# Performance work log

Measured on AMD Instinct MI355X. Metric: run time of the kernel, lower is better.

Reference implementation:

```python
import jax, jax.numpy as jnp
from jax import lax
import numpy as np

B, C, T = 128, 64, 750
NOUT, K, HID = 4, 16, 128


def _conv(x, w, b=None):
    y = lax.conv_general_dilated(x, w, (1, 1), 'VALID', dimension_numbers=('NCHW', 'OIHW', 'NCHW'))
    return y if b is None else y + b[None, :, None, None]


def _bn(x, g, b, m, v):
    s = g / jnp.sqrt(v + 1e-5)
    return (x - m[None, :, None, None]) * s[None, :, None, None] + b[None, :, None, None]


def _pool(x):
    return lax.reduce_window(x, -jnp.inf, lax.max, (1, 1, 3, 1), (1, 1, 3, 1), 'VALID')


def _backbone(x, ct_w, ct_b, cs_w, bn1, c2_w, bn2, c3_w, bn3, c4_w, bn4, fc_w, fc_b):
    # x: (B, C, T) -> (B, 1, T, C)  (braindecode transpose_time_to_spat)
    h = jnp.transpose(x, (0, 2, 1))[:, None]
    h = _conv(h, ct_w, ct_b)              # (B,25,T-9,C)
    h = _conv(h, cs_w)                    # (B,25,T-9,1)
    h = _pool(jax.nn.elu(_bn(h, *bn1)))   # (B,25,247,1)
    h = _pool(jax.nn.elu(_bn(_conv(h, c2_w), *bn2)))  # (B,50,79,1)
    h = _pool(jax.nn.elu(_bn(_conv(h, c3_w), *bn3)))  # (B,100,23,1)
    h = _pool(jax.nn.elu(_bn(_conv(h, c4_w), *bn4)))  # (B,200,4,1)
    h = _conv(h, fc_w, fc_b)              # (B,NOUT,1,1)
    return h[:, :, 0, 0]                  # (B,NOUT)


def _heads(feats, cluster_ids, hW1, hb1, hW2, hb2):
    # gather per-sample head params, batched small GEMMs (MoE-style dispatch)
    h = jax.nn.relu(jnp.einsum('bf,bfh->bh', feats, hW1[cluster_ids]) + hb1[cluster_ids])
    return jnp.einsum('bh,bho->bo', h, hW2[cluster_ids]) + hb2[cluster_ids]


def setup_inputs() -> dict:
    key = jax.random.key(0)
    ks = jax.random.split(key, 40)
    n = lambda i, shape, s=0.1: jax.random.normal(ks[i], shape, dtype=jnp.float32) * s
    u = lambda i, shape: jax.random.uniform(ks[i], shape, dtype=jnp.float32) + 0.5
    inp = {
        'x': n(0, (B, C, T), 1.0),
        'cluster_ids': jax.random.randint(ks[1], (B,), 0, K),
        'ct_w': n(2, (25, 1, 10, 1)), 'ct_b': n(3, (25,)),
        'cs_w': n(4, (25, 25, 1, C)),
        'bn1_g': u(5, (25,)), 'bn1_b': n(6, (25,)), 'bn1_m': n(7, (25,)), 'bn1_v': u(8, (25,)),
        'c2_w': n(9, (50, 25, 10, 1)),
        'bn2_g': u(10, (50,)), 'bn2_b': n(11, (50,)), 'bn2_m': n(12, (50,)), 'bn2_v': u(13, (50,)),
        'c3_w': n(14, (100, 50, 10, 1)),
        'bn3_g': u(15, (100,)), 'bn3_b': n(16, (100,)), 'bn3_m': n(17, (100,)), 'bn3_v': u(18, (100,)),
        'c4_w': n(19, (200, 100, 10, 1)),
        'bn4_g': u(20, (200,)), 'bn4_b': n(21, (200,)), 'bn4_m': n(22, (200,)), 'bn4_v': u(23, (200,)),
        'fc_w': n(24, (NOUT, 200, 4, 1)), 'fc_b': n(25, (NOUT,)),
        'hW1': n(26, (K, NOUT, HID)), 'hb1': n(27, (K, HID)),
        'hW2': n(28, (K, HID, NOUT)), 'hb2': n(29, (K, NOUT)),
    }
    return inp


def reference(x, cluster_ids, ct_w, ct_b, cs_w,
              bn1_g, bn1_b, bn1_m, bn1_v, c2_w,
              bn2_g, bn2_b, bn2_m, bn2_v, c3_w,
              bn3_g, bn3_b, bn3_m, bn3_v, c4_w,
              bn4_g, bn4_b, bn4_m, bn4_v, fc_w, fc_b,
              hW1, hb1, hW2, hb2):
    feats = _backbone(x, ct_w, ct_b, cs_w,
                      (bn1_g, bn1_b, bn1_m, bn1_v), c2_w,
                      (bn2_g, bn2_b, bn2_m, bn2_v), c3_w,
                      (bn3_g, bn3_b, bn3_m, bn3_v), c4_w,
                      (bn4_g, bn4_b, bn4_m, bn4_v), fc_w, fc_b)
    return _heads(feats, cluster_ids, hW1, hb1, hW2, hb2)
```

## Files before the change

### kernel.cpp

```cpp
#include <hip/hip_runtime.h>
#include <hip/hip_bf16.h>
#include <math.h>

typedef __attribute__((ext_vector_type(8))) short short8v;
typedef __attribute__((ext_vector_type(4))) float f32x4;

#define F_S1 0
#define F_H1 32
#define F_S2 64
#define F_H2 128
#define F_S3 192
#define F_H3 320
#define F_S4 448
#define F_H4 704
#define F_B1 960
#define F_P4 1024
#define F_END (1024 + 128*200*4)
#define H_BASE (F_END*2)
#define H_P1  H_BASE
#define H_WA1 (H_P1 + 128*8192)
#define H_WA2 (H_WA1 + 32*640)
#define H_WA3 (H_WA2 + 64*320)
#define H_WA4 (H_WA3 + 112*640)
#define H_P2  (H_WA4 + 208*1280)
#define H_P3  (H_P2 + 79*128*64)

#define N_WA1 (32*640)
#define N_WA2 (64*320)
#define N_WA3 (112*640)
#define N_WA4 (208*1280)
#define N_WTOT (N_WA1 + N_WA2 + N_WA3 + N_WA4)

__device__ __forceinline__ float eluf(float v) {
    return v > 0.f ? v : (expf(v) - 1.f);
}
__device__ __forceinline__ float ldh(const __hip_bfloat16* p) { return __bfloat162float(*p); }
__device__ __forceinline__ unsigned short bfb(float v) {
    __hip_bfloat16 h = __float2bfloat16(v);
    return reinterpret_cast<unsigned short&>(h);
}
__device__ __forceinline__ void ld4f(const float* p, float* v) {
    float2 a = *(const float2*)p, c = *(const float2*)(p + 2);
    v[0] = a.x; v[1] = a.y; v[2] = c.x; v[3] = c.y;
}

__global__ __launch_bounds__(256) void k_pre2(
    const float* __restrict__ ct_w, const float* __restrict__ ct_b,
    const float* __restrict__ cs_w,
    const float* __restrict__ g1, const float* __restrict__ b1,
    const float* __restrict__ m1, const float* __restrict__ v1,
    const float* __restrict__ w2,
    const float* __restrict__ g2, const float* __restrict__ b2,
    const float* __restrict__ m2, const float* __restrict__ v2,
    const float* __restrict__ w3,
    const float* __restrict__ g3, const float* __restrict__ b3,
    const float* __restrict__ m3, const float* __restrict__ v3,
    const float* __restrict__ w4,
    const float* __restrict__ g4, const float* __restrict__ b4,
    const float* __restrict__ m4, const float* __restrict__ v4,
    float* __restrict__ ws) {
    __hip_bfloat16* wsh = (__hip_bfloat16*)ws;
    int t = blockIdx.x * 256 + threadIdx.x;
    if (t < N_WA1) {
        int o = t / 640, kv = t - o * 640, kk = kv / 64, c = kv - kk * 64;
        float s = 0.f;
        if (o < 25)
            for (int i = 0; i < 25; ++i)
                s += cs_w[(o * 25 + i) * 64 + c] * ct_w[i * 10 + kk];
        wsh[H_WA1 + t] = __float2bfloat16(s);
    } else if (t < N_WA1 + N_WA2) {
        int u = t - N_WA1;
        int o = u / 320, kv = u - o * 320, kk = kv / 32, c = kv - kk * 32;
        float s = (o < 50 && c < 25) ? w2[(o * 25 + c) * 10 + kk] : 0.f;
        wsh[H_WA2 + u] = __float2bfloat16(s);
    } else if (t < N_WA1 + N_WA2 + N_WA3) {
        int u = t - N_WA1 - N_WA2;
        int o = u / 640, kv = u - o * 640, kk = kv / 64, c = kv - kk * 64;
        float s = (o < 100 && c < 50) ? w3[(o * 50 + c) * 10 + kk] : 0.f;
        wsh[H_WA3 + u] = __float2bfloat16(s);
    } else if (t < N_WTOT) {
        int u = t - N_WA1 - N_WA2 - N_WA3;
        int o = u / 1280, kv = u - o * 1280, kk = kv / 128, c = kv - kk * 128;
        float s = (o < 200 && c < 100) ? w4[(o * 100 + c) * 10 + kk] : 0.f;
        wsh[H_WA4 + u] = __float2bfloat16(s);
    } else {
        int j = t - N_WTOT;
        if (j < 25) {
            float sc = g1[j] / sqrtf(v1[j] + 1e-5f);
            ws[F_S1 + j] = sc; ws[F_H1 + j] = b1[j] - m1[j] * sc;
        } else if (j >= 32 && j < 82) {
            int ch = j - 32;
            float sc = g2[ch] / sqrtf(v2[ch] + 1e-5f);
            ws[F_S2 + ch] = sc; ws[F_H2 + ch] = b2[ch] - m2[ch] * sc;
        } else if (j >= 96 && j < 196) {
            int ch = j - 96;
            float sc = g3[ch] / sqrtf(v3[ch] + 1e-5f);
            ws[F_S3 + ch] = sc; ws[F_H3 + ch] = b3[ch] - m3[ch] * sc;
        } else if (j >= 224 && j < 424) {
            int ch = j - 224;
            float sc = g4[ch] / sqrtf(v4[ch] + 1e-5f);
            ws[F_S4 + ch] = sc; ws[F_H4 + ch] = b4[ch] - m4[ch] * sc;
        } else if (j >= 448 && j < 473) {
            int o = j - 448;
            float s = 0.f;
            for (int i = 0; i < 25; ++i) {
                float cs = 0.f;
                for (int c = 0; c < 64; ++c) cs += cs_w[(o * 25 + i) * 64 + c];
                s += cs * ct_b[i];
            }
            ws[F_B1 + o] = s;
        }
    }
}

__global__ __launch_bounds__(256) void k_conv1(
    const float* __restrict__ x, float* __restrict__ ws) {
    __hip_bfloat16* wsh = (__hip_bfloat16*)ws;
    const __hip_bfloat16* Wa = wsh + H_WA1;
    int bx = blockIdx.x, b = blockIdx.y;
    int tp0 = bx * 42;
    int PTb = min(42, 247 - tp0);
    int t0 = 126 * bx;

    __shared__ __align__(16) __hip_bfloat16 xb[144 * 64];
    __shared__ __align__(16) __hip_bfloat16 eb[32 * 128];

    for (int f = threadIdx.x; f < 64 * 36; f += 256) {
        int c = f / 36, j = f - c * 36;
        int t = t0 + 4 * j;
        const float* src = x + ((size_t)b * 64 + c) * 750 + t;
        float v[4];
        if (t + 3 < 750) {
            ld4f(src, v);
        } else {
#pragma unroll
            for (int e = 0; e < 4; ++e) v[e] = (t + e < 750) ? src[e] : 0.f;
        }
#pragma unroll
        for (int e = 0; e < 4; ++e) {
            int r = 4 * j + e;
            xb[r * 64 + (c ^ (8 * (r & 7)))] = __float2bfloat16(v[e]);
        }
    }
    __syncthreads();

    int lane = threadIdx.x & 63, wid = threadIdx.x >> 6;
    int lo = lane & 15, kg = lane >> 4;
    int ot = wid >> 1, ctg = wid & 1;
    const short8v* Ap = (const short8v*)(Wa + (size_t)(ot * 16 + lo) * 640);
    f32x4 acc[4];
#pragma unroll
    for (int q = 0; q < 4; ++q) acc[q] = (f32x4){0.f, 0.f, 0.f, 0.f};
#pragma unroll 1
    for (int sb = 0; sb < 20; sb += 10) {
        short8v af[10];
#pragma unroll
        for (int u = 0; u < 10; ++u) af[u] = Ap[(sb + u) * 4 + kg];
#pragma unroll
        for (int u = 0; u < 10; ++u) {
            int s = sb + u;
            int kk = s >> 1, cb = s & 1;
#pragma unroll
            for (int q = 0; q < 4; ++q) {
                int r = (ctg * 4 + q) * 16 + lo + kk;
                int cs = (cb * 32 + kg * 8) ^ (8 * (r & 7));
                short8v bf = *(const short8v*)&xb[r * 64 + cs];
                acc[q] = __builtin_amdgcn_mfma_f32_16x16x32_bf16(af[u], bf, acc[q], 0, 0, 0);
            }
        }
    }
#pragma unroll
    for (int q = 0; q < 4; ++q) {
        int tloc = (ctg * 4 + q) * 16 + lo;
#pragma unroll
        for (int e = 0; e < 4; ++e) {
            int o2 = ot * 16 + kg * 4 + e;
            float a = acc[q][e] + ws[F_B1 + o2];
            eb[o2 * 128 + tloc] = __float2bfloat16(eluf(a * ws[F_S1 + o2] + ws[F_H1 + o2]));
        }
    }
    __syncthreads();

    __hip_bfloat16* p1g = wsh + H_P1;
    for (int i = threadIdx.x; i < 8 * 42; i += 256) {
        int og = i / 42, pl = i - og * 42;
        if (pl < PTb) {
            int tp = tp0 + pl;
            unsigned short uv[4];
#pragma unroll
            for (int j = 0; j < 4; ++j) {
                int o = og * 4 + j;
                float v = 0.f;
                if (o < 25) {
                    const __hip_bfloat16* ep = eb + o * 128 + 3 * pl;
                    v = fmaxf(fmaxf(ldh(ep), ldh(ep + 1)), ldh(ep + 2));
                }
                uv[j] = bfb(v);
            }
            uint2 pk = {(unsigned)uv[0] | ((unsigned)uv[1] << 16),
                        (unsigned)uv[2] | ((unsigned)uv[3] << 16)};
            *(uint2*)(p1g + (size_t)tp * 4096 + b * 32 + og * 4) = pk;
        }
    }
}

__global__ __launch_bounds__(256) void k_gemm2(float* __restrict__ ws) {
    __hip_bfloat16* wsh = (__hip_bfloat16*)ws;
    const __hip_bfloat16* p1 = wsh + H_P1;
    const __hip_bfloat16* W = wsh + H_WA2;
    __hip_bfloat16* p2 = wsh + H_P2;
    int w = blockIdx.x * 4 + (threadIdx.x >> 6);
    int lane = threadIdx.x & 63, lo = lane & 15, kg = lane >> 4;
    int tp = w >> 3, s0 = (w & 7) * 16;

    const __hip_bfloat16* bbase = p1 + (size_t)(s0 + lo) * 32 + kg * 8;
    short8v B[12];
#pragma unroll
    for (int v = 0; v < 12; ++v)
        B[v] = *(const short8v*)(bbase + (size_t)(3 * tp + v) * 4096);

    f32x4 acc[4][3];
#pragma unroll
    for (int ot = 0; ot < 4; ++ot)
#pragma unroll
        for (int u = 0; u < 3; ++u) acc[ot][u] = (f32x4){0.f, 0.f, 0.f, 0.f};

#pragma unroll
    for (int ot = 0; ot < 4; ++ot) {
        const __hip_bfloat16* arow = W + (size_t)(ot * 16 + lo) * 320 + kg * 8;
#pragma unroll
        for (int kk = 0; kk < 10; ++kk) {
            short8v a = *(const short8v*)(arow + kk * 32);
#pragma unroll
            for (int u = 0; u < 3; ++u)
                acc[ot][u] = __builtin_amdgcn_mfma_f32_16x16x32_bf16(a, B[kk + u], acc[ot][u], 0, 0, 0);
        }
    }

    __hip_bfloat16* obase = p2 + (size_t)(tp * 128 + s0 + lo) * 64;
#pragma unroll
    for (int ot = 0; ot < 4; ++ot) {
        unsigned short uv[4];
#pragma unroll
        for (int e = 0; e < 4; ++e) {
            int o2 = ot * 16 + kg * 4 + e;
            float m = fmaxf(fmaxf(acc[ot][0][e], acc[ot][1][e]), acc[ot][2][e]);
            float val = (o2 < 50) ? eluf(m * ws[F_S2 + o2] + ws[F_H2 + o2]) : 0.f;
            uv[e] = bfb(val);
        }
        uint2 pk = {(unsigned)uv[0] | ((unsigned)uv[1] << 16),
                    (unsigned)uv[2] | ((unsigned)uv[3] << 16)};
        *(uint2*)(obase + ot * 16 + kg * 4) = pk;
    }
}

__global__ __launch_bounds__(256) void k_gemm3(float* __restrict__ ws) {
    __hip_bfloat16* wsh = (__hip_bfloat16*)ws;
    const __hip_bfloat16* p2 = wsh + H_P2;
    const __hip_bfloat16* W = wsh + H_WA3;
    __hip_bfloat16* p3 = wsh + H_P3;
    int w = blockIdx.x * 4 + (threadIdx.x >> 6);
    int lane = threadIdx.x & 63, lo = lane & 15, kg = lane >> 4;
    int col = w >> 1, oz = w & 1;
    int tp = col >> 3, s0 = (col & 7) * 16;

    const __hip_bfloat16* bbase = p2 + (size_t)(s0 + lo) * 64 + kg * 8;
    f32x4 acc[4][3];
#pragma unroll
    for (int ot = 0; ot < 4; ++ot)
#pragma unroll
        for (int u = 0; u < 3; ++u) acc[ot][u] = (f32x4){0.f, 0.f, 0.f, 0.f};

#pragma unroll
    for (int cb = 0; cb < 2; ++cb) {
        short8v B[12];
#pragma unroll
        for (int v = 0; v < 12; ++v)
            B[v] = *(const short8v*)(bbase + (size_t)(3 * tp + v) * 8192 + cb * 32);
#pragma unroll
        for (int ot = 0; ot < 4; ++ot) {
            if (oz && ot == 3) continue;
            const __hip_bfloat16* arow =
                W + (size_t)(oz * 64 + ot * 16 + lo) * 640 + cb * 32 + kg * 8;
#pragma unroll
            for (int kk = 0; kk < 10; ++kk) {
                short8v a = *(const short8v*)(arow + kk * 64);
#pragma unroll
                for (int u = 0; u < 3; ++u)
                    acc[ot][u] = __builtin_amdgcn_mfma_f32_16x16x32_bf16(a, B[kk + u], acc[ot][u], 0, 0, 0);
            }
        }
    }

    __hip_bfloat16* obase = p3 + (size_t)(tp * 128 + s0 + lo) * 128;
#pragma unroll
    for (int ot = 0; ot < 4; ++ot) {
        unsigned short uv[4];
#pragma unroll
        for (int e = 0; e < 4; ++e) {
            int o2 = oz * 64 + ot * 16 + kg * 4 + e;
            float val = 0.f;
            if (o2 < 100) {
                float m = fmaxf(fmaxf(acc[ot][0][e], acc[ot][1][e]), acc[ot][2][e]);
                val = eluf(m * ws[F_S3 + o2] + ws[F_H3 + o2]);
            }
            uv[e] = bfb(val);
        }
        uint2 pk = {(unsigned)uv[0] | ((unsigned)uv[1] << 16),
                    (unsigned)uv[2] | ((unsigned)uv[3] << 16)};
        *(uint2*)(obase + oz * 64 + ot * 16 + kg * 4) = pk;
    }
}

__global__ __launch_bounds__(256) void k_gemm4(float* __restrict__ ws) {
    __hip_bfloat16* wsh = (__hip_bfloat16*)ws;
    const __hip_bfloat16* p3 = wsh + H_P3;
    const __hip_bfloat16* W = wsh + H_WA4;
    float* p4 = ws + F_P4;
    int w = blockIdx.x * 4 + (threadIdx.x >> 6);
    int lane = threadIdx.x & 63, lo = lane & 15, kg = lane >> 4;
    int ot = w >> 5, ct = w & 31;
    int tp = ct >> 3, s0 = (ct & 7) * 16;

    const __hip_bfloat16* bbase = p3 + (size_t)(s0 + lo) * 128 + kg * 8;
    const __hip_bfloat16* arow0 = W + (size_t)(ot * 16 + lo) * 1280 + kg * 8;
    f32x4 acc[3];
#pragma unroll
    for (int u = 0; u < 3; ++u) acc[u] = (f32x4){0.f, 0.f, 0.f, 0.f};

#pragma unroll
    for (int cb = 0; cb < 4; ++cb) {
        short8v B[12];
#pragma unroll
        for (int v = 0; v < 12; ++v)
            B[v] = *(const short8v*)(bbase + (size_t)(3 * tp + v) * 16384 + cb * 32);
        const __hip_bfloat16* arow = arow0 + cb * 32;
#pragma unroll
        for (int kk = 0; kk < 10; ++kk) {
            short8v a = *(const short8v*)(arow + kk * 128);
#pragma unroll
            for (int u = 0; u < 3; ++u)
                acc[u] = __builtin_amdgcn_mfma_f32_16x16x32_bf16(a, B[kk + u], acc[u], 0, 0, 0);
        }
    }

#pragma unroll
    for (int e = 0; e < 4; ++e) {
        int o2 = ot * 16 + kg * 4 + e;
        if (o2 < 200) {
            float m = fmaxf(fmaxf(acc[0][e], acc[1][e]), acc[2][e]);
            p4[((size_t)(s0 + lo) * 200 + o2) * 4 + tp] =
                eluf(m * ws[F_S4 + o2] + ws[F_H4 + o2]);
        }
    }
}

__global__ __launch_bounds__(128) void k_heads(
    const float* __restrict__ ws,
    const float* __restrict__ fcw, const float* __restrict__ fcb,
    const int* __restrict__ cids,
    const float* __restrict__ hW1, const float* __restrict__ hb1,
    const float* __restrict__ hW2, const float* __restrict__ hb2,
    float* __restrict__ out) {
    const float* p4 = ws + F_P4;
    __shared__ float red[4][128];
    __shared__ float fs[4];
    int b = blockIdx.x, j = threadIdx.x;

    float pa[4] = {0.f, 0.f, 0.f, 0.f};
    for (int c = j; c < 200; c += 128) {
        const float* pp = p4 + ((size_t)b * 200 + c) * 4;
        float v0 = pp[0], v1 = pp[1], v2 = pp[2], v3 = pp[3];
#pragma unroll
        for (int o = 0; o < 4; ++o) {
            const float* fw = fcw + (o * 200 + c) * 4;
            pa[o] += fw[0] * v0 + fw[1] * v1 + fw[2] * v2 + fw[3] * v3;
        }
    }
#pragma unroll
    for (int o = 0; o < 4; ++o) red[o][j] = pa[o];
    __syncthreads();
    for (int s = 64; s > 0; s >>= 1) {
        if (j < s) {
#pragma unroll
            for (int o = 0; o < 4; ++o) red[o][j] += red[o][j + s];
        }
        __syncthreads();
    }
    if (j < 4) fs[j] = red[j][0] + fcb[j];
    __syncthreads();

    int cid = cids[b];
    float hvv = hb1[cid * 128 + j];
#pragma unroll
    for (int f = 0; f < 4; ++f) hvv += fs[f] * hW1[(cid * 4 + f) * 128 + j];
    hvv = fmaxf(hvv, 0.f);
#pragma unroll
    for (int o = 0; o < 4; ++o) red[o][j] = hvv * hW2[(cid * 128 + j) * 4 + o];
    __syncthreads();
    for (int s = 64; s > 0; s >>= 1) {
        if (j < s) {
#pragma unroll
            for (int o = 0; o < 4; ++o) red[o][j] += red[o][j + s];
        }
        __syncthreads();
    }
    if (j < 4) out[b * 4 + j] = red[j][0] + hb2[cid * 4 + j];
}

extern "C" void kernel_launch(void* const* d_in, const int* in_sizes, int n_in,
                              void* d_out, int out_size, void* d_ws, size_t ws_size,
                              hipStream_t stream) {
    (void)in_sizes; (void)n_in; (void)out_size; (void)ws_size;
    const float* x    = (const float*)d_in[0];
    const int*   cid  = (const int*)d_in[1];
    const float* ctw  = (const float*)d_in[2];
    const float* ctb  = (const float*)d_in[3];
    const float* csw  = (const float*)d_in[4];
    const float* g1 = (const float*)d_in[5],  *b1 = (const float*)d_in[6];
    const float* m1 = (const float*)d_in[7],  *v1 = (const float*)d_in[8];
    const float* w2 = (const float*)d_in[9];
    const float* g2 = (const float*)d_in[10], *b2 = (const float*)d_in[11];
    const float* m2 = (const float*)d_in[12], *v2 = (const float*)d_in[13];
    const float* w3 = (const float*)d_in[14];
    const float* g3 = (const float*)d_in[15], *b3 = (const float*)d_in[16];
    const float* m3 = (const float*)d_in[17], *v3 = (const float*)d_in[18];
    const float* w4 = (const float*)d_in[19];
    const float* g4 = (const float*)d_in[20], *b4 = (const float*)d_in[21];
    const float* m4 = (const float*)d_in[22], *v4 = (const float*)d_in[23];
    const float* fcw = (const float*)d_in[24], *fcb = (const float*)d_in[25];
    const float* hW1 = (const float*)d_in[26], *hb1 = (const float*)d_in[27];
    const float* hW2 = (const float*)d_in[28], *hb2 = (const float*)d_in[29];
    float* ws  = (float*)d_ws;
    float* out = (float*)d_out;

    k_pre2<<<dim3((N_WTOT + 512 + 255) / 256), dim3(256), 0, stream>>>(
        ctw, ctb, csw, g1, b1, m1, v1, w2, g2, b2, m2, v2,
        w3, g3, b3, m3, v3, w4, g4, b4, m4, v4, ws);
    k_conv1<<<dim3(6, 128), dim3(256), 0, stream>>>(x, ws);
    k_gemm2<<<dim3(158), dim3(256), 0, stream>>>(ws);
    k_gemm3<<<dim3(92),  dim3(256), 0, stream>>>(ws);
    k_gemm4<<<dim3(104), dim3(256), 0, stream>>>(ws);
    k_heads<<<dim3(128), dim3(128), 0, stream>>>(ws, fcw, fcb, cid,
                                                 hW1, hb1, hW2, hb2, out);
}
```

Before: 95.93 us.

## Fuse weight prep into conv1, split gemm2 finer, fold heads into gemm4

Merges the weight-prep kernel and conv1 into one launch: conv blocks rebuild the combined temporal-spatial conv1 weights in shared memory, while extra blocks convert the later-layer weights. Gemm2 now has each wave compute two output tiles, which doubles the block count. The FC and MoE heads are folded into gemm4 through a last-block-done atomic counter. The goal is to cut launch count and serial dependencies, at the cost of every conv block recomputing the conv1 weights and the heads running on a single block.

Result: slower. 151.7 us (+58.1%).

```diff
diff --git a/kernel.cpp b/kernel.cpp
--- a/kernel.cpp
+++ b/kernel.cpp
@@ -5,31 +5,30 @@
 typedef __attribute__((ext_vector_type(8))) short short8v;
 typedef __attribute__((ext_vector_type(4))) float f32x4;
 
-#define F_S1 0
-#define F_H1 32
 #define F_S2 64
 #define F_H2 128
 #define F_S3 192
 #define F_H3 320
 #define F_S4 448
 #define F_H4 704
-#define F_B1 960
+#define F_BAR 1008
 #define F_P4 1024
 #define F_END (1024 + 128*200*4)
 #define H_BASE (F_END*2)
 #define H_P1  H_BASE
-#define H_WA1 (H_P1 + 128*8192)
-#define H_WA2 (H_WA1 + 32*640)
+#define H_WA2 (H_P1 + 128*8192)
 #define H_WA3 (H_WA2 + 64*320)
 #define H_WA4 (H_WA3 + 112*640)
 #define H_P2  (H_WA4 + 208*1280)
 #define H_P3  (H_P2 + 79*128*64)
 
-#define N_WA1 (32*640)
 #define N_WA2 (64*320)
 #define N_WA3 (112*640)
 #define N_WA4 (208*1280)
-#define N_WTOT (N_WA1 + N_WA2 + N_WA3 + N_WA4)
+#define N234  (N_WA2 + N_WA3 + N_WA4)
+
+#define CONV_BLOCKS 768
+#define CVT_BLOCKS  1402
 
 __device__ __forceinline__ float eluf(float v) {
     return v > 0.f ? v : (expf(v) - 1.f);
@@ -44,7 +43,8 @@
     v[0] = a.x; v[1] = a.y; v[2] = c.x; v[3] = c.y;
 }
 
-__global__ __launch_bounds__(256) void k_pre2(
+__global__ __launch_bounds__(256) void k_front(
+    const float* __restrict__ x,
     const float* __restrict__ ct_w, const float* __restrict__ ct_b,
     const float* __restrict__ cs_w,
     const float* __restrict__ g1, const float* __restrict__ b1,
@@ -60,72 +60,94 @@
     const float* __restrict__ m4, const float* __restrict__ v4,
     float* __restrict__ ws) {
     __hip_bfloat16* wsh = (__hip_bfloat16*)ws;
-    int t = blockIdx.x * 256 + threadIdx.x;
-    if (t < N_WA1) {
-        int o = t / 640, kv = t - o * 640, kk = kv / 64, c = kv - kk * 64;
-        float s = 0.f;
-        if (o < 25)
-            for (int i = 0; i < 25; ++i)
-                s += cs_w[(o * 25 + i) * 64 + c] * ct_w[i * 10 + kk];
-        wsh[H_WA1 + t] = __float2bfloat16(s);
-    } else if (t < N_WA1 + N_WA2) {
-        int u = t - N_WA1;
-        int o = u / 320, kv = u - o * 320, kk = kv / 32, c = kv - kk * 32;
-        float s = (o < 50 && c < 25) ? w2[(o * 25 + c) * 10 + kk] : 0.f;
-        wsh[H_WA2 + u] = __float2bfloat16(s);
-    } else if (t < N_WA1 + N_WA2 + N_WA3) {
-        int u = t - N_WA1 - N_WA2;
-        int o = u / 640, kv = u - o * 640, kk = kv / 64, c = kv - kk * 64;
-        float s = (o < 100 && c < 50) ? w3[(o * 50 + c) * 10 + kk] : 0.f;
-        wsh[H_WA3 + u] = __float2bfloat16(s);
-    } else if (t < N_WTOT) {
-        int u = t - N_WA1 - N_WA2 - N_WA3;
-        int o = u / 1280, kv = u - o * 1280, kk = kv / 128, c = kv - kk * 128;
-        float s = (o < 200 && c < 100) ? w4[(o * 100 + c) * 10 + kk] : 0.f;
-        wsh[H_WA4 + u] = __float2bfloat16(s);
-    } else {
-        int j = t - N_WTOT;
-        if (j < 25) {
-            float sc = g1[j] / sqrtf(v1[j] + 1e-5f);
-            ws[F_S1 + j] = sc; ws[F_H1 + j] = b1[j] - m1[j] * sc;
-        } else if (j >= 32 && j < 82) {
-            int ch = j - 32;
-            float sc = g2[ch] / sqrtf(v2[ch] + 1e-5f);
-            ws[F_S2 + ch] = sc; ws[F_H2 + ch] = b2[ch] - m2[ch] * sc;
-        } else if (j >= 96 && j < 196) {
-            int ch = j - 96;
-            float sc = g3[ch] / sqrtf(v3[ch] + 1e-5f);
-            ws[F_S3 + ch] = sc; ws[F_H3 + ch] = b3[ch] - m3[ch] * sc;
-        } else if (j >= 224 && j < 424) {
-            int ch = j - 224;
-            float sc = g4[ch] / sqrtf(v4[ch] + 1e-5f);
-            ws[F_S4 + ch] = sc; ws[F_H4 + ch] = b4[ch] - m4[ch] * sc;
-        } else if (j >= 448 && j < 473) {
-            int o = j - 448;
+    int bx = blockIdx.x, tid = threadIdx.x;
+
+    if (bx >= CONV_BLOCKS) {
+        if (bx == CONV_BLOCKS && tid == 0) {
+            unsigned* cnt = (unsigned*)(ws + F_BAR);
+            __hip_atomic_store(cnt, 0u, __ATOMIC_RELAXED, __HIP_MEMORY_SCOPE_AGENT);
+        }
+        int u = (bx - CONV_BLOCKS) * 256 + tid;
+        if (u < N_WA2) {
+            int o = u / 320, kv = u - o * 320, kk = kv / 32, c = kv - kk * 32;
+            float s = (o < 50 && c < 25) ? w2[(o * 25 + c) * 10 + kk] : 0.f;
+            wsh[H_WA2 + u] = __float2bfloat16(s);
+        } else if (u < N_WA2 + N_WA3) {
+            int v = u - N_WA2;
+            int o = v / 640, kv = v - o * 640, kk = kv / 64, c = kv - kk * 64;
+            float s = (o < 100 && c < 50) ? w3[(o * 50 + c) * 10 + kk] : 0.f;
+            wsh[H_WA3 + v] = __float2bfloat16(s);
+        } else if (u < N234) {
+            int v = u - N_WA2 - N_WA3;
+            int o = v / 1280, kv = v - o * 1280, kk = kv / 128, c = kv - kk * 128;
+            float s = (o < 200 && c < 100) ? w4[(o * 100 + c) * 10 + kk] : 0.f;
+            wsh[H_WA4 + v] = __float2bfloat16(s);
+        } else {
+            int j = u - N234;
+            if (j < 50) {
+                float sc = g2[j] / sqrtf(v2[j] + 1e-5f);
+                ws[F_S2 + j] = sc; ws[F_H2 + j] = b2[j] - m2[j] * sc;
+            } else if (j >= 64 && j < 164) {
+                int ch = j - 64;
+                float sc = g3[ch] / sqrtf(v3[ch] + 1e-5f);
+                ws[F_S3 + ch] = sc; ws[F_H3 + ch] = b3[ch] - m3[ch] * sc;
+            } else if (j >= 192 && j < 392) {
+                int ch = j - 192;
+                float sc = g4[ch] / sqrtf(v4[ch] + 1e-5f);
+                ws[F_S4 + ch] = sc; ws[F_H4 + ch] = b4[ch] - m4[ch] * sc;
+            }
+        }
+        return;
+    }
+
+    int b = bx / 6, sub = bx % 6;
+    int tp0 = sub * 42;
+    int PTb = min(42, 247 - tp0);
+    int t0 = 126 * sub;
+    int lane = tid & 63, wid = tid >> 6;
+    int lo = lane & 15, kg = lane >> 4;
+
+    __shared__ __align__(16) __hip_bfloat16 wa1[32 * 640];
+    __shared__ __align__(16) __hip_bfloat16 xb[144 * 64];
+    __shared__ float ctl[250];
+    __shared__ float ctbl[25];
+    __shared__ float s1l[32], h1l[32], b1l[32];
+    __hip_bfloat16* eb = xb;
+
+    if (tid < 250) ctl[tid] = ct_w[tid];
+    if (tid >= 256 - 25) ctbl[tid - (256 - 25)] = ct_b[tid - (256 - 25)];
+    if (tid < 32) {
+        b1l[tid] = 0.f;
+        float sc = 0.f, hh = 0.f;
+        if (tid < 25) {
+            sc = g1[tid] / sqrtf(v1[tid] + 1e-5f);
+            hh = b1[tid] - m1[tid] * sc;
+        }
+        s1l[tid] = sc; h1l[tid] = hh;
+    }
+    for (int e = tid; e < 7 * 640; e += 256)
+        wa1[25 * 640 + e] = __float2bfloat16(0.f);
+    __syncthreads();
+
+    for (int p = tid; p < 1600; p += 256) {
+        int o = p >> 6, c = p & 63;
+        float cw[25];
+#pragma unroll
+        for (int i = 0; i < 25; ++i) cw[i] = cs_w[(o * 25 + i) * 64 + c];
+        float tb = 0.f;
+#pragma unroll
+        for (int i = 0; i < 25; ++i) tb += cw[i] * ctbl[i];
+        atomicAdd(&b1l[o], tb);
+        int omask = 8 * (o & 7);
+#pragma unroll
+        for (int kk = 0; kk < 10; ++kk) {
             float s = 0.f;
-            for (int i = 0; i < 25; ++i) {
-                float cs = 0.f;
-                for (int c = 0; c < 64; ++c) cs += cs_w[(o * 25 + i) * 64 + c];
-                s += cs * ct_b[i];
-            }
-            ws[F_B1 + o] = s;
-        }
-    }
-}
-
-__global__ __launch_bounds__(256) void k_conv1(
-    const float* __restrict__ x, float* __restrict__ ws) {
-    __hip_bfloat16* wsh = (__hip_bfloat16*)ws;
-    const __hip_bfloat16* Wa = wsh + H_WA1;
-    int bx = blockIdx.x, b = blockIdx.y;
-    int tp0 = bx * 42;
-    int PTb = min(42, 247 - tp0);
-    int t0 = 126 * bx;
-
-    __shared__ __align__(16) __hip_bfloat16 xb[144 * 64];
-    __shared__ __align__(16) __hip_bfloat16 eb[32 * 128];
-
-    for (int f = threadIdx.x; f < 64 * 36; f += 256) {
+#pragma unroll
+            for (int i = 0; i < 25; ++i) s += cw[i] * ctl[i * 10 + kk];
+            wa1[o * 640 + ((kk * 64 + c) ^ omask)] = __float2bfloat16(s);
+        }
+    }
+    for (int f = tid; f < 64 * 36; f += 256) {
         int c = f / 36, j = f - c * 36;
         int t = t0 + 4 * j;
         const float* src = x + ((size_t)b * 64 + c) * 750 + t;
@@ -144,10 +166,9 @@
     }
     __syncthreads();
 
-    int lane = threadIdx.x & 63, wid = threadIdx.x >> 6;
-    int lo = lane & 15, kg = lane >> 4;
     int ot = wid >> 1, ctg = wid & 1;
-    const short8v* Ap = (const short8v*)(Wa + (size_t)(ot * 16 + lo) * 640);
+    const __hip_bfloat16* Arow = wa1 + (ot * 16 + lo) * 640;
+    int amask = 8 * (lo & 7);
     f32x4 acc[4];
 #pragma unroll
     for (int q = 0; q < 4; ++q) acc[q] = (f32x4){0.f, 0.f, 0.f, 0.f};
@@ -155,7 +176,8 @@
     for (int sb = 0; sb < 20; sb += 10) {
         short8v af[10];
 #pragma unroll
-        for (int u = 0; u < 10; ++u) af[u] = Ap[(sb + u) * 4 + kg];
+        for (int u = 0; u < 10; ++u)
+            af[u] = *(const short8v*)&Arow[(((sb + u) * 32 + kg * 8)) ^ amask];
 #pragma unroll
         for (int u = 0; u < 10; ++u) {
             int s = sb + u;
@@ -169,21 +191,23 @@
             }
         }
     }
+    __syncthreads();
+
 #pragma unroll
     for (int q = 0; q < 4; ++q) {
         int tloc = (ctg * 4 + q) * 16 + lo;
 #pragma unroll
         for (int e = 0; e < 4; ++e) {
             int o2 = ot * 16 + kg * 4 + e;
-            float a = acc[q][e] + ws[F_B1 + o2];
-            eb[o2 * 128 + tloc] = __float2bfloat16(eluf(a * ws[F_S1 + o2] + ws[F_H1 + o2]));
+            float a = acc[q][e] + b1l[o2];
+            eb[o2 * 128 + tloc] = __float2bfloat16(eluf(a * s1l[o2] + h1l[o2]));
         }
     }
     __syncthreads();
 
     __hip_bfloat16* p1g = wsh + H_P1;
-    for (int i = threadIdx.x; i < 8 * 42; i += 256) {
-        int og = i / 42, pl = i - og * 42;
+    for (int i = tid; i < 42 * 8; i += 256) {
+        int pl = i >> 3, og = i & 7;
         if (pl < PTb) {
             int tp = tp0 + pl;
             unsigned short uv[4];
@@ -211,46 +235,38 @@
     __hip_bfloat16* p2 = wsh + H_P2;
     int w = blockIdx.x * 4 + (threadIdx.x >> 6);
     int lane = threadIdx.x & 63, lo = lane & 15, kg = lane >> 4;
-    int tp = w >> 3, s0 = (w & 7) * 16;
+    int otp = w & 1, cw = w >> 1;
+    int tp = cw >> 3, s0 = (cw & 7) * 16;
 
     const __hip_bfloat16* bbase = p1 + (size_t)(s0 + lo) * 32 + kg * 8;
     short8v B[12];
 #pragma unroll
     for (int v = 0; v < 12; ++v)
         B[v] = *(const short8v*)(bbase + (size_t)(3 * tp + v) * 4096);
-
-    f32x4 acc[4][3];
-#pragma unroll
-    for (int ot = 0; ot < 4; ++ot)
-#pragma unroll
-        for (int u = 0; u < 3; ++u) acc[ot][u] = (f32x4){0.f, 0.f, 0.f, 0.f};
-
-#pragma unroll
-    for (int ot = 0; ot < 4; ++ot) {
+#pragma unroll
+    for (int oi = 0; oi < 2; ++oi) {
+        int ot = otp * 2 + oi;
+        f32x4 acc[3];
+#pragma unroll
+        for (int u = 0; u < 3; ++u) acc[u] = (f32x4){0.f, 0.f, 0.f, 0.f};
         const __hip_bfloat16* arow = W + (size_t)(ot * 16 + lo) * 320 + kg * 8;
 #pragma unroll
         for (int kk = 0; kk < 10; ++kk) {
             short8v a = *(const short8v*)(arow + kk * 32);
 #pragma unroll
             for (int u = 0; u < 3; ++u)
-                acc[ot][u] = __builtin_amdgcn_mfma_f32_16x16x32_bf16(a, B[kk + u], acc[ot][u], 0, 0, 0);
-        }
-    }
-
-    __hip_bfloat16* obase = p2 + (size_t)(tp * 128 + s0 + lo) * 64;
-#pragma unroll
-    for (int ot = 0; ot < 4; ++ot) {
+                acc[u] = __builtin_amdgcn_mfma_f32_16x16x32_bf16(a, B[kk + u], acc[u], 0, 0, 0);
+        }
         unsigned short uv[4];
 #pragma unroll
         for (int e = 0; e < 4; ++e) {
             int o2 = ot * 16 + kg * 4 + e;
-            float m = fmaxf(fmaxf(acc[ot][0][e], acc[ot][1][e]), acc[ot][2][e]);
-            float val = (o2 < 50) ? eluf(m * ws[F_S2 + o2] + ws[F_H2 + o2]) : 0.f;
-            uv[e] = bfb(val);
+            float m = fmaxf(fmaxf(acc[0][e], acc[1][e]), acc[2][e]);
+            uv[e] = bfb((o2 < 50) ? eluf(m * ws[F_S2 + o2] + ws[F_H2 + o2]) : 0.f);
         }
         uint2 pk = {(unsigned)uv[0] | ((unsigned)uv[1] << 16),
                     (unsigned)uv[2] | ((unsigned)uv[3] << 16)};
-        *(uint2*)(obase + ot * 16 + kg * 4) = pk;
+        *(uint2*)(p2 + (size_t)(tp * 128 + s0 + lo) * 64 + ot * 16 + kg * 4) = pk;
     }
 }
 
@@ -312,100 +328,98 @@
     }
 }
 
-__global__ __launch_bounds__(256) void k_gemm4(float* __restrict__ ws) {
+__global__ __launch_bounds__(256) void k_gemm4h(
+    float* __restrict__ ws, const int* __restrict__ cids,
+    const float* __restrict__ fcw, const float* __restrict__ fcb,
+    const float* __restrict__ hW1, const float* __restrict__ hb1,
+    const float* __restrict__ hW2, const float* __restrict__ hb2,
+    float* __restrict__ out) {
     __hip_bfloat16* wsh = (__hip_bfloat16*)ws;
     const __hip_bfloat16* p3 = wsh + H_P3;
     const __hip_bfloat16* W = wsh + H_WA4;
     float* p4 = ws + F_P4;
-    int w = blockIdx.x * 4 + (threadIdx.x >> 6);
-    int lane = threadIdx.x & 63, lo = lane & 15, kg = lane >> 4;
-    int ot = w >> 5, ct = w & 31;
-    int tp = ct >> 3, s0 = (ct & 7) * 16;
-
-    const __hip_bfloat16* bbase = p3 + (size_t)(s0 + lo) * 128 + kg * 8;
-    const __hip_bfloat16* arow0 = W + (size_t)(ot * 16 + lo) * 1280 + kg * 8;
-    f32x4 acc[3];
-#pragma unroll
-    for (int u = 0; u < 3; ++u) acc[u] = (f32x4){0.f, 0.f, 0.f, 0.f};
-
-#pragma unroll
-    for (int cb = 0; cb < 4; ++cb) {
-        short8v B[12];
-#pragma unroll
-        for (int v = 0; v < 12; ++v)
-            B[v] = *(const short8v*)(bbase + (size_t)(3 * tp + v) * 16384 + cb * 32);
-        const __hip_bfloat16* arow = arow0 + cb * 32;
-#pragma unroll
-        for (int kk = 0; kk < 10; ++kk) {
-            short8v a = *(const short8v*)(arow + kk * 128);
-#pragma unroll
-            for (int u = 0; u < 3; ++u)
-                acc[u] = __builtin_amdgcn_mfma_f32_16x16x32_bf16(a, B[kk + u], acc[u], 0, 0, 0);
-        }
-    }
-
-#pragma unroll
-    for (int e = 0; e < 4; ++e) {
-        int o2 = ot * 16 + kg * 4 + e;
-        if (o2 < 200) {
-            float m = fmaxf(fmaxf(acc[0][e], acc[1][e]), acc[2][e]);
-            p4[((size_t)(s0 + lo) * 200 + o2) * 4 + tp] =
-                eluf(m * ws[F_S4 + o2] + ws[F_H4 + o2]);
-        }
-    }
-}
-
-__global__ __launch_bounds__(128) void k_heads(
-    const float* __restrict__ ws,
-    const float* __restrict__ fcw, const float* __restrict__ fcb,
-    const int* __restrict__ cids,
-    const float* __restrict__ hW1, const float* __restrict__ hb1,
-    const float* __restrict__ hW2, const float* __restrict__ hb2,
-    float* __restrict__ out) {
-    const float* p4 = ws + F_P4;
-    __shared__ float red[4][128];
-    __shared__ float fs[4];
-    int b = blockIdx.x, j = threadIdx.x;
-
-    float pa[4] = {0.f, 0.f, 0.f, 0.f};
-    for (int c = j; c < 200; c += 128) {
-        const float* pp = p4 + ((size_t)b * 200 + c) * 4;
-        float v0 = pp[0], v1 = pp[1], v2 = pp[2], v3 = pp[3];
-#pragma unroll
-        for (int o = 0; o < 4; ++o) {
-            const float* fw = fcw + (o * 200 + c) * 4;
-            pa[o] += fw[0] * v0 + fw[1] * v1 + fw[2] * v2 + fw[3] * v3;
-        }
-    }
-#pragma unroll
-    for (int o = 0; o < 4; ++o) red[o][j] = pa[o];
-    __syncthreads();
-    for (int s = 64; s > 0; s >>= 1) {
-        if (j < s) {
-#pragma unroll
-            for (int o = 0; o < 4; ++o) red[o][j] += red[o][j + s];
-        }
-        __syncthreads();
-    }
-    if (j < 4) fs[j] = red[j][0] + fcb[j];
-    __syncthreads();
-
-    int cid = cids[b];
-    float hvv = hb1[cid * 128 + j];
-#pragma unroll
-    for (int f = 0; f < 4; ++f) hvv += fs[f] * hW1[(cid * 4 + f) * 128 + j];
-    hvv = fmaxf(hvv, 0.f);
-#pragma unroll
-    for (int o = 0; o < 4; ++o) red[o][j] = hvv * hW2[(cid * 128 + j) * 4 + o];
-    __syncthreads();
-    for (int s = 64; s > 0; s >>= 1) {
-        if (j < s) {
-#pragma unroll
-            for (int o = 0; o < 4; ++o) red[o][j] += red[o][j + s];
-        }
-        __syncthreads();
-    }
-    if (j < 4) out[b * 4 + j] = red[j][0] + hb2[cid * 4 + j];
+    int tid = threadIdx.x;
+    int w = blockIdx.x * 4 + (tid >> 6);
+    int lane = tid & 63, lo = lane & 15, kg = lane >> 4;
+    {
+        int ot = w >> 5, ct = w & 31;
+        int tp = ct >> 3, s0 = (ct & 7) * 16;
+        const __hip_bfloat16* bbase = p3 + (size_t)(s0 + lo) * 128 + kg * 8;
+        const __hip_bfloat16* arow0 = W + (size_t)(ot * 16 + lo) * 1280 + kg * 8;
+        f32x4 acc[3];
+#pragma unroll
+        for (int u = 0; u < 3; ++u) acc[u] = (f32x4){0.f, 0.f, 0.f, 0.f};
+#pragma unroll
+        for (int cb = 0; cb < 4; ++cb) {
+            short8v B[12];
+#pragma unroll
+            for (int v = 0; v < 12; ++v)
+                B[v] = *(const short8v*)(bbase + (size_t)(3 * tp + v) * 16384 + cb * 32);
+            const __hip_bfloat16* arow = arow0 + cb * 32;
+#pragma unroll
+            for (int kk = 0; kk < 10; ++kk) {
+                short8v a = *(const short8v*)(arow + kk * 128);
+#pragma unroll
+                for (int u = 0; u < 3; ++u)
+                    acc[u] = __builtin_amdgcn_mfma_f32_16x16x32_bf16(a, B[kk + u], acc[u], 0, 0, 0);
+            }
+        }
+#pragma unroll
+        for (int e = 0; e < 4; ++e) {
+            int o2 = ot * 16 + kg * 4 + e;
+            if (o2 < 200) {
+                float m = fmaxf(fmaxf(acc[0][e], acc[1][e]), acc[2][e]);
+                p4[((size_t)(s0 + lo) * 200 + o2) * 4 + tp] =
+                    eluf(m * ws[F_S4 + o2] + ws[F_H4 + o2]);
+            }
+        }
+    }
+
+    __shared__ unsigned lastFlag;
+    __syncthreads();
+    if (tid == 0) {
+        unsigned* cnt = (unsigned*)(ws + F_BAR);
+        unsigned v = __hip_atomic_fetch_add(cnt, 1u, __ATOMIC_ACQ_REL,
+                                            __HIP_MEMORY_SCOPE_AGENT);
+        lastFlag = (v == 103u);
+    }
+    __syncthreads();
+    if (!lastFlag) return;
+
+    int s = tid >> 1, half = tid & 1;
+    const float* pp = p4 + (size_t)s * 800 + half * 400;
+    float fcv[4] = {0.f, 0.f, 0.f, 0.f};
+    for (int c = 0; c < 100; ++c) {
+        const float* q = pp + c * 4;
+        float v0 = q[0], v1 = q[1], v2 = q[2], v3 = q[3];
+        int cg = half * 100 + c;
+#pragma unroll
+        for (int oo = 0; oo < 4; ++oo) {
+            const float* fw = fcw + (oo * 200 + cg) * 4;
+            fcv[oo] += fw[0] * v0 + fw[1] * v1 + fw[2] * v2 + fw[3] * v3;
+        }
+    }
+    float fc[4];
+#pragma unroll
+    for (int oo = 0; oo < 4; ++oo)
+        fc[oo] = fcv[oo] + __shfl_xor(fcv[oo], 1) + fcb[oo];
+
+    int cid = cids[s];
+    float o4[4] = {0.f, 0.f, 0.f, 0.f};
+    for (int h = half * 64; h < half * 64 + 64; ++h) {
+        float hv = hb1[cid * 128 + h];
+#pragma unroll
+        for (int f = 0; f < 4; ++f) hv += fc[f] * hW1[(cid * 4 + f) * 128 + h];
+        hv = fmaxf(hv, 0.f);
+#pragma unroll
+        for (int oo = 0; oo < 4; ++oo) o4[oo] += hv * hW2[(cid * 128 + h) * 4 + oo];
+    }
+#pragma unroll
+    for (int oo = 0; oo < 4; ++oo) o4[oo] += __shfl_xor(o4[oo], 1);
+    if (!half) {
+#pragma unroll
+        for (int oo = 0; oo < 4; ++oo) out[s * 4 + oo] = o4[oo] + hb2[cid * 4 + oo];
+    }
 }
 
 extern "C" void kernel_launch(void* const* d_in, const int* in_sizes, int n_in,
@@ -434,13 +448,11 @@
     float* ws  = (float*)d_ws;
     float* out = (float*)d_out;
 
-    k_pre2<<<dim3((N_WTOT + 512 + 255) / 256), dim3(256), 0, stream>>>(
-        ctw, ctb, csw, g1, b1, m1, v1, w2, g2, b2, m2, v2,
+    k_front<<<dim3(CONV_BLOCKS + CVT_BLOCKS), dim3(256), 0, stream>>>(
+        x, ctw, ctb, csw, g1, b1, m1, v1, w2, g2, b2, m2, v2,
         w3, g3, b3, m3, v3, w4, g4, b4, m4, v4, ws);
-    k_conv1<<<dim3(6, 128), dim3(256), 0, stream>>>(x, ws);
-    k_gemm2<<<dim3(158), dim3(256), 0, stream>>>(ws);
+    k_gemm2<<<dim3(316), dim3(256), 0, stream>>>(ws);
     k_gemm3<<<dim3(92),  dim3(256), 0, stream>>>(ws);
-    k_gemm4<<<dim3(104), dim3(256), 0, stream>>>(ws);
-    k_heads<<<dim3(128), dim3(128), 0, stream>>>(ws, fcw, fcb, cid,
-                                                 hW1, hb1, hW2, hb2, out);
-}
+    k_gemm4h<<<dim3(104), dim3(256), 0, stream>>>(ws, cid, fcw, fcb,
+                                                  hW1, hb1, hW2, hb2, out);
+}
```
